# Optimization experiments

Hardware: AMD Instinct MI355X
Metric: run time of the kernel (lower is better)

The kernel has to match this reference:

```python
import jax, jax.numpy as jnp
import numpy as np

V, E, H = 32000, 512, 512  # output_dim, emb_dim, hid_dim
B, S = 256, 128


def setup_inputs() -> dict:
    key = jax.random.key(0)
    ks = jax.random.split(key, 16)
    d = {
        'input_ids': jax.random.randint(ks[0], (B,), 0, V),
        'encoded': jax.random.normal(ks[1], (B, S, 2 * H), jnp.float32),
        'src': jax.random.randint(ks[2], (B, S), 0, V),
        'prev_state': jax.random.normal(ks[3], (B, H), jnp.float32),
        'weighted': jax.random.normal(ks[4], (B, 2 * H), jnp.float32),
        'order': 1,
        # parameters (PyTorch layouts: Linear weight is (out,in); GRU gates order r,z,n)
        'embed_w': jax.random.normal(ks[5], (V, E), jnp.float32) * 0.02,
        'gru_w_ih': jax.random.normal(ks[6], (3 * H, E + 2 * H), jnp.float32) * 0.02,
        'gru_w_hh': jax.random.normal(ks[7], (3 * H, H), jnp.float32) * 0.02,
        'gru_b_ih': jnp.zeros((3 * H,), jnp.float32),
        'gru_b_hh': jnp.zeros((3 * H,), jnp.float32),
        'Ws_w': jax.random.normal(ks[8], (H, 2 * H), jnp.float32) * 0.02,
        'Ws_b': jnp.zeros((H,), jnp.float32),
        'Wo_w': jax.random.normal(ks[9], (V, H), jnp.float32) * 0.02,
        'Wo_b': jnp.zeros((V,), jnp.float32),
        'Wc_w': jax.random.normal(ks[10], (H, 2 * H), jnp.float32) * 0.02,
        'Wc_b': jnp.zeros((H,), jnp.float32),
    }
    return d


def _forward(input_ids, encoded, src, prev_state, weighted, order,
             embed_w, gru_w_ih, gru_w_hh, gru_b_ih, gru_b_hh,
             Ws_w, Ws_b, Wo_w, Wo_b, Wc_w, Wc_b):
    b, s, _ = encoded.shape
    v = Wo_w.shape[0]
    if order == 0:
        prev_state = encoded[:, -1] @ Ws_w.T + Ws_b           # (B,H)
        weighted = jnp.zeros((b, 2 * gru_w_hh.shape[1]), encoded.dtype)
    # GRU cell, single step (seq_len=1), torch gate order r,z,n
    x = jnp.concatenate([embed_w[input_ids], weighted], axis=-1)  # (B, E+2H)
    gi = x @ gru_w_ih.T + gru_b_ih
    gh = prev_state @ gru_w_hh.T + gru_b_hh
    i_r, i_z, i_n = jnp.split(gi, 3, axis=-1)
    h_r, h_z, h_n = jnp.split(gh, 3, axis=-1)
    r = jax.nn.sigmoid(i_r + h_r)
    z = jax.nn.sigmoid(i_z + h_z)
    n = jnp.tanh(i_n + r * h_n)
    hidden = (1.0 - z) * n + z * prev_state                    # (B,H)

    score_g = hidden @ Wo_w.T + Wo_b                           # (B,V)
    score_c = jnp.tanh(encoded @ Wc_w.T + Wc_b)                # (B,S,H)
    score_c = jnp.einsum('bsh,bh->bs', score_c, hidden)        # (B,S)
    mask = (src == 0).astype(encoded.dtype) * -1000.0
    score_c = jnp.tanh(score_c + mask)

    probs = jax.nn.softmax(jnp.concatenate([score_g, score_c], axis=1), axis=1)
    prob_g = probs[:, :v]
    prob_c = probs[:, v:]                                      # (B,S)

    # vectorized scatter-add replacing the nested python loops
    rows = jnp.arange(b)[:, None]
    prob_c_to_g = jnp.zeros((b, v), probs.dtype).at[rows, src].add(prob_c)
    predicted = (prob_g + prob_c_to_g)[:, None, :]             # (B,1,V)

    eq = (src == input_ids[:, None]).astype(encoded.dtype)     # (B,S)
    idx = eq / jnp.maximum(eq.sum(axis=1, keepdims=True), 1.0)
    attn = prob_c * idx                                        # (B,S)
    weighted_out = jnp.einsum('bs,bsd->bd', attn, encoded)     # (B,2H)
    return predicted, hidden, weighted_out


def reference(input_ids, encoded, src, prev_state, weighted, order,
              embed_w, gru_w_ih, gru_w_hh, gru_b_ih, gru_b_hh,
              Ws_w, Ws_b, Wo_w, Wo_b, Wc_w, Wc_b):
    return _forward(input_ids, encoded, src, prev_state, weighted, order,
                    embed_w, gru_w_ih, gru_w_hh, gru_b_ih, gru_b_hh,
                    Ws_w, Ws_b, Wo_w, Wo_b, Wc_w, Wc_b)
```

## Files before the change

kernel.cpp:

```cpp
#include <hip/hip_runtime.h>
#include <cstdint>
#include <cstddef>

#define B_ 256
#define S_ 128
#define H_ 512
#define E_ 512
#define V_ 32000
#define NBLK_G (V_ / 64)

typedef _Float16 half_t;
typedef _Float16 half8 __attribute__((ext_vector_type(8)));
typedef float floatx4 __attribute__((ext_vector_type(4)));

__device__ __forceinline__ float sigmoidf_(float x) { return 1.0f / (1.0f + __expf(-x)); }
__device__ __forceinline__ float fast_tanh(float x) {
    float e = __expf(2.0f * x);
    return 1.0f - 2.0f / (e + 1.0f);
}

__global__ __launch_bounds__(256)
void prep_kernel(const int* __restrict__ ids, const float* __restrict__ encoded,
                 const float* __restrict__ prev_state, const float* __restrict__ weighted,
                 const int* __restrict__ order_p, const float* __restrict__ embed,
                 const float* __restrict__ Ws_w, const float* __restrict__ Ws_b,
                 float* __restrict__ x, float* __restrict__ prev)
{
    int i = blockIdx.x * 256 + threadIdx.x;
    int b = i >> 11;
    int j = i & 2047;
    int order = order_p[0];
    if (j < 1536) {
        float v;
        if (j < 512) v = embed[(size_t)ids[b] * E_ + j];
        else         v = (order == 0) ? 0.0f : weighted[b * 1024 + (j - 512)];
        x[b * 1536 + j] = v;
    } else {
        int h = j - 1536;
        float v;
        if (order != 0) {
            v = prev_state[b * H_ + h];
        } else {
            const float* e  = encoded + ((size_t)b * S_ + (S_ - 1)) * 1024;
            const float* wr = Ws_w + (size_t)h * 1024;
            float accv = Ws_b[h];
            for (int k = 0; k < 1024; ++k) accv += e[k] * wr[k];
            v = accv;
        }
        prev[b * H_ + h] = v;
    }
}

template<int BM, int BN, int WAVES_M, int WAVES_N, int EPI>
__global__ __launch_bounds__(256, 2)
void gemm_f16(const float* __restrict__ A, const float* __restrict__ Bw,
              float* __restrict__ C, const float* __restrict__ bias,
              float* __restrict__ aux, int K, int lda, int ldb, int ldc, int nblk)
{
    constexpr int BK = 32;
    constexpr int WM = BM / WAVES_M;
    constexpr int WN = BN / WAVES_N;
    constexpr int FM = WM / 16;
    constexpr int FN = WN / 16;
    constexpr int A_ITEMS = (BM * 4) / 256;
    constexpr int B_ITEMS = (BN * 4) / 256;

    __shared__ half_t As[BM * BK];
    __shared__ half_t Bs[BN * BK];

    const int tid  = threadIdx.x;
    const int wid  = tid >> 6;
    const int lane = tid & 63;
    const int wm   = wid % WAVES_M;
    const int wn   = wid / WAVES_M;
    const int bm0  = blockIdx.y * BM;
    const int bn0  = blockIdx.x * BN;
    const int col  = lane & 15;
    const int quad = lane >> 4;
    const int swz  = (quad ^ (col & 3)) * 8;

    floatx4 acc[FM][FN] = {};

    for (int kt = 0; kt < K; kt += BK) {
        float4 ar[A_ITEMS][2], br[B_ITEMS][2];
#pragma unroll
        for (int i = 0; i < A_ITEMS; ++i) {
            int idx = tid + i * 256, row = idx >> 2, ch = idx & 3;
            const float* p = A + (size_t)(bm0 + row) * lda + kt + ch * 8;
            ar[i][0] = *(const float4*)p; ar[i][1] = *(const float4*)(p + 4);
        }
#pragma unroll
        for (int i = 0; i < B_ITEMS; ++i) {
            int idx = tid + i * 256, row = idx >> 2, ch = idx & 3;
            const float* p = Bw + (size_t)(bn0 + row) * ldb + kt + ch * 8;
            br[i][0] = *(const float4*)p; br[i][1] = *(const float4*)(p + 4);
        }
        __syncthreads();
#pragma unroll
        for (int i = 0; i < A_ITEMS; ++i) {
            int idx = tid + i * 256, row = idx >> 2, ch = idx & 3;
            int pos = (ch ^ (row & 3)) * 8;
            half8 h;
            h[0] = (half_t)ar[i][0].x; h[1] = (half_t)ar[i][0].y;
            h[2] = (half_t)ar[i][0].z; h[3] = (half_t)ar[i][0].w;
            h[4] = (half_t)ar[i][1].x; h[5] = (half_t)ar[i][1].y;
            h[6] = (half_t)ar[i][1].z; h[7] = (half_t)ar[i][1].w;
            *(half8*)(&As[row * BK + pos]) = h;
        }
#pragma unroll
        for (int i = 0; i < B_ITEMS; ++i) {
            int idx = tid + i * 256, row = idx >> 2, ch = idx & 3;
            int pos = (ch ^ (row & 3)) * 8;
            half8 h;
            h[0] = (half_t)br[i][0].x; h[1] = (half_t)br[i][0].y;
            h[2] = (half_t)br[i][0].z; h[3] = (half_t)br[i][0].w;
            h[4] = (half_t)br[i][1].x; h[5] = (half_t)br[i][1].y;
            h[6] = (half_t)br[i][1].z; h[7] = (half_t)br[i][1].w;
            *(half8*)(&Bs[row * BK + pos]) = h;
        }
        __syncthreads();

        half8 af[FM], bf[FN];
#pragma unroll
        for (int fm = 0; fm < FM; ++fm)
            af[fm] = *(const half8*)(&As[(wm * WM + fm * 16 + col) * BK + swz]);
#pragma unroll
        for (int fn = 0; fn < FN; ++fn)
            bf[fn] = *(const half8*)(&Bs[(wn * WN + fn * 16 + col) * BK + swz]);
#pragma unroll
        for (int fm = 0; fm < FM; ++fm)
#pragma unroll
            for (int fn = 0; fn < FN; ++fn)
                acc[fm][fn] = __builtin_amdgcn_mfma_f32_16x16x32_f16(af[fm], bf[fn], acc[fm][fn], 0, 0, 0);
    }

    if constexpr (EPI == 0) {
#pragma unroll
        for (int fm = 0; fm < FM; ++fm) {
            int m0 = bm0 + wm * WM + fm * 16 + quad * 4;
#pragma unroll
            for (int fn = 0; fn < FN; ++fn) {
                int n = bn0 + wn * WN + fn * 16 + col;
                float bv = bias[n];
#pragma unroll
                for (int r = 0; r < 4; ++r)
                    C[(size_t)(m0 + r) * ldc + n] = acc[fm][fn][r] + bv;
            }
        }
    } else {
        const int bx = blockIdx.x;
#pragma unroll
        for (int fm = 0; fm < FM; ++fm) {
            int m0 = bm0 + wm * WM + fm * 16 + quad * 4;
            float vv[FN][4];
#pragma unroll
            for (int fn = 0; fn < FN; ++fn) {
                int n = bn0 + fn * 16 + col;
                float bv = bias[n];
#pragma unroll
                for (int r = 0; r < 4; ++r) {
                    vv[fn][r] = acc[fm][fn][r] + bv;
                    C[(size_t)(m0 + r) * ldc + n] = vv[fn][r];
                }
            }
#pragma unroll
            for (int r = 0; r < 4; ++r) {
                float mx = vv[0][r];
#pragma unroll
                for (int fn = 1; fn < FN; ++fn) mx = fmaxf(mx, vv[fn][r]);
#pragma unroll
                for (int off = 1; off < 16; off <<= 1)
                    mx = fmaxf(mx, __shfl_xor(mx, off, 64));
                float se = 0.f;
#pragma unroll
                for (int fn = 0; fn < FN; ++fn) se += __expf(vv[fn][r] - mx);
#pragma unroll
                for (int off = 1; off < 16; off <<= 1)
                    se += __shfl_xor(se, off, 64);
                if (col == 0) {
                    aux[(size_t)(m0 + r) * nblk + bx] = mx;
                    aux[(size_t)256 * nblk + (size_t)(m0 + r) * nblk + bx] = se;
                }
            }
        }
    }
}

__global__ __launch_bounds__(512, 2)
void wc_sc_kernel(const float* __restrict__ enc, const float* __restrict__ Wc,
                  const float* __restrict__ bias, const float* __restrict__ hidden,
                  float* __restrict__ sc_out)
{
    constexpr int BK = 32;
    __shared__ half_t As[64 * BK];
    __shared__ half_t Bs[512 * BK];
    __shared__ float  s_part[4 * 64];

    const int tid  = threadIdx.x;
    const int wid  = tid >> 6;
    const int lane = tid & 63;
    const int wm   = wid & 1;
    const int wn   = wid >> 1;
    const int bm0  = blockIdx.x * 64;
    const int col  = lane & 15;
    const int quad = lane >> 4;
    const int swz  = (quad ^ (col & 3)) * 8;

    floatx4 acc[2][8] = {};

    for (int kt = 0; kt < 1024; kt += BK) {
        float4 br[4][2], ar[2];
#pragma unroll
        for (int i = 0; i < 4; ++i) {
            int idx = tid + i * 512, row = idx >> 2, ch = idx & 3;
            const float* p = Wc + (size_t)row * 1024 + kt + ch * 8;
            br[i][0] = *(const float4*)p; br[i][1] = *(const float4*)(p + 4);
        }
        if (tid < 256) {
            int row = tid >> 2, ch = tid & 3;
            const float* p = enc + (size_t)(bm0 + row) * 1024 + kt + ch * 8;
            ar[0] = *(const float4*)p; ar[1] = *(const float4*)(p + 4);
        }
        __syncthreads();
#pragma unroll
        for (int i = 0; i < 4; ++i) {
            int idx = tid + i * 512, row = idx >> 2, ch = idx & 3;
            int pos = (ch ^ (row & 3)) * 8;
            half8 h;
            h[0] = (half_t)br[i][0].x; h[1] = (half_t)br[i][0].y;
            h[2] = (half_t)br[i][0].z; h[3] = (half_t)br[i][0].w;
            h[4] = (half_t)br[i][1].x; h[5] = (half_t)br[i][1].y;
            h[6] = (half_t)br[i][1].z; h[7] = (half_t)br[i][1].w;
            *(half8*)(&Bs[row * BK + pos]) = h;
        }
        if (tid < 256) {
            int row = tid >> 2, ch = tid & 3;
            int pos = (ch ^ (row & 3)) * 8;
            half8 h;
            h[0] = (half_t)ar[0].x; h[1] = (half_t)ar[0].y;
            h[2] = (half_t)ar[0].z; h[3] = (half_t)ar[0].w;
            h[4] = (half_t)ar[1].x; h[5] = (half_t)ar[1].y;
            h[6] = (half_t)ar[1].z; h[7] = (half_t)ar[1].w;
            *(half8*)(&As[row * BK + pos]) = h;
        }
        __syncthreads();

        half8 af[2], bf[8];
#pragma unroll
        for (int fm = 0; fm < 2; ++fm)
            af[fm] = *(const half8*)(&As[(wm * 32 + fm * 16 + col) * BK + swz]);
#pragma unroll
        for (int fn = 0; fn < 8; ++fn)
            bf[fn] = *(const half8*)(&Bs[(wn * 128 + fn * 16 + col) * BK + swz]);
#pragma unroll
        for (int fm = 0; fm < 2; ++fm)
#pragma unroll
            for (int fn = 0; fn < 8; ++fn)
                acc[fm][fn] = __builtin_amdgcn_mfma_f32_16x16x32_f16(af[fm], bf[fn], acc[fm][fn], 0, 0, 0);
    }

    const float* hid = hidden + (size_t)(bm0 >> 7) * H_;
#pragma unroll
    for (int fm = 0; fm < 2; ++fm) {
        float p0 = 0.f, p1 = 0.f, p2 = 0.f, p3 = 0.f;
#pragma unroll
        for (int fn = 0; fn < 8; ++fn) {
            int n = wn * 128 + fn * 16 + col;
            float bv = bias[n];
            float hv = hid[n];
            p0 += fast_tanh(acc[fm][fn][0] + bv) * hv;
            p1 += fast_tanh(acc[fm][fn][1] + bv) * hv;
            p2 += fast_tanh(acc[fm][fn][2] + bv) * hv;
            p3 += fast_tanh(acc[fm][fn][3] + bv) * hv;
        }
#pragma unroll
        for (int off = 1; off < 16; off <<= 1) {
            p0 += __shfl_xor(p0, off, 64);
            p1 += __shfl_xor(p1, off, 64);
            p2 += __shfl_xor(p2, off, 64);
            p3 += __shfl_xor(p3, off, 64);
        }
        if (col == 0) {
            int rloc = wm * 32 + fm * 16 + quad * 4;
            s_part[wn * 64 + rloc + 0] = p0;
            s_part[wn * 64 + rloc + 1] = p1;
            s_part[wn * 64 + rloc + 2] = p2;
            s_part[wn * 64 + rloc + 3] = p3;
        }
    }
    __syncthreads();
    if (tid < 64) {
        float s = s_part[tid] + s_part[64 + tid] + s_part[128 + tid] + s_part[192 + tid];
        sc_out[bm0 + tid] = s;
    }
}

__global__ __launch_bounds__(256)
void gate_kernel(const float* __restrict__ gi, const float* __restrict__ gh,
                 const float* __restrict__ prev, float* __restrict__ hidden)
{
    int i = blockIdx.x * 256 + threadIdx.x;
    int b = i >> 9;
    int h = i & 511;
    const float* gib = gi + (size_t)b * 1536;
    const float* ghb = gh + (size_t)b * 1536;
    float r = sigmoidf_(gib[h] + ghb[h]);
    float z = sigmoidf_(gib[h + 512] + ghb[h + 512]);
    float n = tanhf(gib[h + 1024] + r * ghb[h + 1024]);
    hidden[i] = (1.0f - z) * n + z * prev[i];
}

__global__ __launch_bounds__(256)
void final_kernel(const float* __restrict__ sc_raw,
                  const int* __restrict__ src, const int* __restrict__ ids,
                  const float* __restrict__ encoded, const float* __restrict__ parts,
                  float* __restrict__ predicted, float* __restrict__ weighted_out)
{
    int b = blockIdx.x;
    int t = threadIdx.x;
    __shared__ float s_scf[S_];
    __shared__ float s_attn[S_];
    __shared__ int   s_src[S_];
    __shared__ float rm[4], rs[4];
    __shared__ int   s_cnt;

    float* pred = predicted + (size_t)b * V_;
    const float* pm = parts + (size_t)b * NBLK_G;
    const float* ps = parts + (size_t)256 * NBLK_G + (size_t)b * NBLK_G;

    if (t < S_) {
        int sv = src[b * S_ + t];
        s_src[t] = sv;
        float raw = sc_raw[b * S_ + t];
        if (sv == 0) raw -= 1000.0f;
        s_scf[t] = tanhf(raw);
    }

    float m = -1e30f, s = 0.f;
    for (int j = t; j < NBLK_G; j += 256) {
        float mo = pm[j], so = ps[j];
        float mn = fmaxf(m, mo);
        s = s * __expf(m - mn) + so * __expf(mo - mn);
        m = mn;
    }
    __syncthreads();
    if (t < S_) {
        float x = s_scf[t];
        float mn = fmaxf(m, x);
        s = s * __expf(m - mn) + __expf(x - mn);
        m = mn;
    }
#pragma unroll
    for (int off = 1; off < 64; off <<= 1) {
        float mo = __shfl_xor(m, off, 64);
        float so = __shfl_xor(s, off, 64);
        float mn = fmaxf(m, mo);
        s = s * __expf(m - mn) + so * __expf(mo - mn);
        m = mn;
    }
    if ((t & 63) == 0) { rm[t >> 6] = m; rs[t >> 6] = s; }
    __syncthreads();
    float M = rm[0], Z = rs[0];
#pragma unroll
    for (int w = 1; w < 4; ++w) {
        float mo = rm[w], so = rs[w];
        float mn = fmaxf(M, mo);
        Z = Z * __expf(M - mn) + so * __expf(mo - mn);
        M = mn;
    }
    float invZ = 1.0f / Z;

    float4* pr4 = (float4*)pred;
    for (int i = t; i < V_ / 4; i += 256) {
        float4 x = pr4[i];
        float4 o;
        o.x = __expf(x.x - M) * invZ;
        o.y = __expf(x.y - M) * invZ;
        o.z = __expf(x.z - M) * invZ;
        o.w = __expf(x.w - M) * invZ;
        pr4[i] = o;
    }

    int ii = ids[b];
    if (t == 0) {
        int c = 0;
        for (int s2 = 0; s2 < S_; ++s2) c += (s_src[s2] == ii) ? 1 : 0;
        s_cnt = (c > 0) ? c : 1;
    }
    __syncthreads();

    if (t < S_) {
        float pc = __expf(s_scf[t] - M) * invZ;
        atomicAdd(&pred[s_src[t]], pc);
        s_attn[t] = (s_src[t] == ii) ? pc / (float)s_cnt : 0.f;
    }
    __syncthreads();

    const float* eb = encoded + (size_t)b * S_ * 1024;
    for (int d = t; d < 1024; d += 256) {
        float accv = 0.f;
        for (int s2 = 0; s2 < S_; ++s2) {
            float a = s_attn[s2];
            if (a != 0.f) accv += a * eb[s2 * 1024 + d];
        }
        weighted_out[b * 1024 + d] = accv;
    }
}

extern "C" void kernel_launch(void* const* d_in, const int* in_sizes, int n_in,
                              void* d_out, int out_size, void* d_ws, size_t ws_size,
                              hipStream_t stream)
{
    const int*   input_ids  = (const int*)d_in[0];
    const float* encoded    = (const float*)d_in[1];
    const int*   src        = (const int*)d_in[2];
    const float* prev_state = (const float*)d_in[3];
    const float* weighted   = (const float*)d_in[4];
    const int*   order      = (const int*)d_in[5];
    const float* embed_w    = (const float*)d_in[6];
    const float* gru_w_ih   = (const float*)d_in[7];
    const float* gru_w_hh   = (const float*)d_in[8];
    const float* gru_b_ih   = (const float*)d_in[9];
    const float* gru_b_hh   = (const float*)d_in[10];
    const float* Ws_w       = (const float*)d_in[11];
    const float* Ws_b       = (const float*)d_in[12];
    const float* Wo_w       = (const float*)d_in[13];
    const float* Wo_b       = (const float*)d_in[14];
    const float* Wc_w       = (const float*)d_in[15];
    const float* Wc_b       = (const float*)d_in[16];
    (void)in_sizes; (void)n_in; (void)out_size; (void)ws_size;

    float* predicted    = (float*)d_out;
    float* hidden       = predicted + (size_t)B_ * V_;
    float* weighted_out = hidden + (size_t)B_ * H_;

    char* w = (char*)d_ws;
    float* x_f32  = (float*)w;  w += (size_t)B_ * 1536 * 4;
    float* prev_f = (float*)w;  w += (size_t)B_ * H_ * 4;
    float* gi     = (float*)w;  w += (size_t)B_ * 1536 * 4;
    float* gh     = (float*)w;  w += (size_t)B_ * 1536 * 4;
    float* sc_raw = (float*)w;  w += (size_t)B_ * S_ * 4;
    float* parts  = (float*)w;  w += (size_t)2 * B_ * NBLK_G * 4;

    prep_kernel<<<2048, 256, 0, stream>>>(input_ids, encoded, prev_state, weighted,
                                          order, embed_w, Ws_w, Ws_b, x_f32, prev_f);

    gemm_f16<64, 64, 2, 2, 0><<<dim3(1536 / 64, 256 / 64), 256, 0, stream>>>(
        x_f32, gru_w_ih, gi, gru_b_ih, nullptr, 1536, 1536, 1536, 1536, 0);
    gemm_f16<64, 64, 2, 2, 0><<<dim3(1536 / 64, 256 / 64), 256, 0, stream>>>(
        prev_f, gru_w_hh, gh, gru_b_hh, nullptr, 512, 512, 512, 1536, 0);

    gate_kernel<<<(B_ * H_) / 256, 256, 0, stream>>>(gi, gh, prev_f, hidden);

    wc_sc_kernel<<<(B_ * S_) / 64, 512, 0, stream>>>(encoded, Wc_w, Wc_b, hidden, sc_raw);

    gemm_f16<256, 64, 4, 1, 2><<<dim3(NBLK_G, 1), 256, 0, stream>>>(
        hidden, Wo_w, predicted, Wo_b, parts, 512, 512, 512, V_, NBLK_G);

    final_kernel<<<B_, 256, 0, stream>>>(sc_raw, src, input_ids, encoded, parts,
                                         predicted, weighted_out);
}
```

Baseline: 507.6 us.

## Pre-convert Wc to fp16 and stream B fragments directly into registers in wc_sc

Adds a small kernel that converts Wc to fp16 once per call into workspace. The wc_sc kernel then loads MFMA B fragments straight from global fp16 memory into registers, so the per-tile fp32 load, conversion and LDS staging of the 512-row weight tile go away. Each wave now owns 64 output columns and all 64 rows. The encoder A tile is double-buffered in LDS with register prefetch, and the occupancy hint is raised. The cost is an extra launch, extra workspace, and B reads from global/L2 that are less coalesced.

```diff
diff --git a/kernel.cpp b/kernel.cpp
--- a/kernel.cpp
+++ b/kernel.cpp
@@ -51,6 +51,19 @@
     }
 }
 
+__global__ __launch_bounds__(256)
+void wc_cvt_kernel(const float* __restrict__ Wc, half_t* __restrict__ out)
+{
+    int i = blockIdx.x * 256 + threadIdx.x;
+    const float* p = Wc + (size_t)i * 8;
+    float4 a = *(const float4*)p;
+    float4 b = *(const float4*)(p + 4);
+    half8 h;
+    h[0] = (half_t)a.x; h[1] = (half_t)a.y; h[2] = (half_t)a.z; h[3] = (half_t)a.w;
+    h[4] = (half_t)b.x; h[5] = (half_t)b.y; h[6] = (half_t)b.z; h[7] = (half_t)b.w;
+    *(half8*)(out + (size_t)i * 8) = h;
+}
+
 template<int BM, int BN, int WAVES_M, int WAVES_N, int EPI>
 __global__ __launch_bounds__(256, 2)
 void gemm_f16(const float* __restrict__ A, const float* __restrict__ Bw,
@@ -186,86 +199,99 @@
     }
 }
 
-__global__ __launch_bounds__(512, 2)
-void wc_sc_kernel(const float* __restrict__ enc, const float* __restrict__ Wc,
+__global__ __launch_bounds__(512, 4)
+void wc_sc_kernel(const float* __restrict__ enc, const half_t* __restrict__ WcH,
                   const float* __restrict__ bias, const float* __restrict__ hidden,
                   float* __restrict__ sc_out)
 {
-    constexpr int BK = 32;
-    __shared__ half_t As[64 * BK];
-    __shared__ half_t Bs[512 * BK];
-    __shared__ float  s_part[4 * 64];
+    __shared__ half_t As[2][64 * 32];
+    __shared__ float  s_part[8 * 64];
 
     const int tid  = threadIdx.x;
     const int wid  = tid >> 6;
     const int lane = tid & 63;
-    const int wm   = wid & 1;
-    const int wn   = wid >> 1;
-    const int bm0  = blockIdx.x * 64;
     const int col  = lane & 15;
     const int quad = lane >> 4;
     const int swz  = (quad ^ (col & 3)) * 8;
-
-    floatx4 acc[2][8] = {};
-
-    for (int kt = 0; kt < 1024; kt += BK) {
-        float4 br[4][2], ar[2];
-#pragma unroll
-        for (int i = 0; i < 4; ++i) {
-            int idx = tid + i * 512, row = idx >> 2, ch = idx & 3;
-            const float* p = Wc + (size_t)row * 1024 + kt + ch * 8;
-            br[i][0] = *(const float4*)p; br[i][1] = *(const float4*)(p + 4);
-        }
+    const int bm0  = blockIdx.x * 64;
+
+    const int ar_row = tid >> 2;
+    const int ar_ch  = tid & 3;
+    const float* aptr = enc + (size_t)(bm0 + ar_row) * 1024 + ar_ch * 8;
+    const int a_pos = ar_row * 32 + (ar_ch ^ (ar_row & 3)) * 8;
+
+    const half_t* bptr0 = WcH + (size_t)(wid * 64 +  0 + col) * 1024 + quad * 8;
+    const half_t* bptr1 = WcH + (size_t)(wid * 64 + 16 + col) * 1024 + quad * 8;
+    const half_t* bptr2 = WcH + (size_t)(wid * 64 + 32 + col) * 1024 + quad * 8;
+    const half_t* bptr3 = WcH + (size_t)(wid * 64 + 48 + col) * 1024 + quad * 8;
+
+    floatx4 acc[4][4] = {};
+    float4 ar0, ar1;
+    half8 bf0[4], bf1[4];
+
+    if (tid < 256) { ar0 = *(const float4*)(aptr); ar1 = *(const float4*)(aptr + 4); }
+    bf0[0] = *(const half8*)(bptr0);
+    bf0[1] = *(const half8*)(bptr1);
+    bf0[2] = *(const half8*)(bptr2);
+    bf0[3] = *(const half8*)(bptr3);
+
+    for (int t2 = 0; t2 < 16; ++t2) {
+        const int kA = t2 * 64;
         if (tid < 256) {
-            int row = tid >> 2, ch = tid & 3;
-            const float* p = enc + (size_t)(bm0 + row) * 1024 + kt + ch * 8;
-            ar[0] = *(const float4*)p; ar[1] = *(const float4*)(p + 4);
+            half8 h;
+            h[0] = (half_t)ar0.x; h[1] = (half_t)ar0.y; h[2] = (half_t)ar0.z; h[3] = (half_t)ar0.w;
+            h[4] = (half_t)ar1.x; h[5] = (half_t)ar1.y; h[6] = (half_t)ar1.z; h[7] = (half_t)ar1.w;
+            *(half8*)(&As[0][a_pos]) = h;
         }
         __syncthreads();
-#pragma unroll
-        for (int i = 0; i < 4; ++i) {
-            int idx = tid + i * 512, row = idx >> 2, ch = idx & 3;
-            int pos = (ch ^ (row & 3)) * 8;
+        if (tid < 256) {
+            ar0 = *(const float4*)(aptr + kA + 32);
+            ar1 = *(const float4*)(aptr + kA + 36);
+        }
+        bf1[0] = *(const half8*)(bptr0 + kA + 32);
+        bf1[1] = *(const half8*)(bptr1 + kA + 32);
+        bf1[2] = *(const half8*)(bptr2 + kA + 32);
+        bf1[3] = *(const half8*)(bptr3 + kA + 32);
+#pragma unroll
+        for (int fm = 0; fm < 4; ++fm) {
+            half8 af = *(const half8*)(&As[0][(fm * 16 + col) * 32 + swz]);
+#pragma unroll
+            for (int fn = 0; fn < 4; ++fn)
+                acc[fm][fn] = __builtin_amdgcn_mfma_f32_16x16x32_f16(af, bf0[fn], acc[fm][fn], 0, 0, 0);
+        }
+        if (tid < 256) {
             half8 h;
-            h[0] = (half_t)br[i][0].x; h[1] = (half_t)br[i][0].y;
-            h[2] = (half_t)br[i][0].z; h[3] = (half_t)br[i][0].w;
-            h[4] = (half_t)br[i][1].x; h[5] = (half_t)br[i][1].y;
-            h[6] = (half_t)br[i][1].z; h[7] = (half_t)br[i][1].w;
-            *(half8*)(&Bs[row * BK + pos]) = h;
-        }
-        if (tid < 256) {
-            int row = tid >> 2, ch = tid & 3;
-            int pos = (ch ^ (row & 3)) * 8;
-            half8 h;
-            h[0] = (half_t)ar[0].x; h[1] = (half_t)ar[0].y;
-            h[2] = (half_t)ar[0].z; h[3] = (half_t)ar[0].w;
-            h[4] = (half_t)ar[1].x; h[5] = (half_t)ar[1].y;
-            h[6] = (half_t)ar[1].z; h[7] = (half_t)ar[1].w;
-            *(half8*)(&As[row * BK + pos]) = h;
+            h[0] = (half_t)ar0.x; h[1] = (half_t)ar0.y; h[2] = (half_t)ar0.z; h[3] = (half_t)ar0.w;
+            h[4] = (half_t)ar1.x; h[5] = (half_t)ar1.y; h[6] = (half_t)ar1.z; h[7] = (half_t)ar1.w;
+            *(half8*)(&As[1][a_pos]) = h;
         }
         __syncthreads();
-
-        half8 af[2], bf[8];
-#pragma unroll
-        for (int fm = 0; fm < 2; ++fm)
-            af[fm] = *(const half8*)(&As[(wm * 32 + fm * 16 + col) * BK + swz]);
-#pragma unroll
-        for (int fn = 0; fn < 8; ++fn)
-            bf[fn] = *(const half8*)(&Bs[(wn * 128 + fn * 16 + col) * BK + swz]);
-#pragma unroll
-        for (int fm = 0; fm < 2; ++fm)
-#pragma unroll
-            for (int fn = 0; fn < 8; ++fn)
-                acc[fm][fn] = __builtin_amdgcn_mfma_f32_16x16x32_f16(af[fm], bf[fn], acc[fm][fn], 0, 0, 0);
+        if (kA + 64 < 1024) {
+            if (tid < 256) {
+                ar0 = *(const float4*)(aptr + kA + 64);
+                ar1 = *(const float4*)(aptr + kA + 68);
+            }
+            bf0[0] = *(const half8*)(bptr0 + kA + 64);
+            bf0[1] = *(const half8*)(bptr1 + kA + 64);
+            bf0[2] = *(const half8*)(bptr2 + kA + 64);
+            bf0[3] = *(const half8*)(bptr3 + kA + 64);
+        }
+#pragma unroll
+        for (int fm = 0; fm < 4; ++fm) {
+            half8 af = *(const half8*)(&As[1][(fm * 16 + col) * 32 + swz]);
+#pragma unroll
+            for (int fn = 0; fn < 4; ++fn)
+                acc[fm][fn] = __builtin_amdgcn_mfma_f32_16x16x32_f16(af, bf1[fn], acc[fm][fn], 0, 0, 0);
+        }
     }
 
     const float* hid = hidden + (size_t)(bm0 >> 7) * H_;
 #pragma unroll
-    for (int fm = 0; fm < 2; ++fm) {
+    for (int fm = 0; fm < 4; ++fm) {
         float p0 = 0.f, p1 = 0.f, p2 = 0.f, p3 = 0.f;
 #pragma unroll
-        for (int fn = 0; fn < 8; ++fn) {
-            int n = wn * 128 + fn * 16 + col;
+        for (int fn = 0; fn < 4; ++fn) {
+            int n = wid * 64 + fn * 16 + col;
             float bv = bias[n];
             float hv = hid[n];
             p0 += fast_tanh(acc[fm][fn][0] + bv) * hv;
@@ -281,16 +307,18 @@
             p3 += __shfl_xor(p3, off, 64);
         }
         if (col == 0) {
-            int rloc = wm * 32 + fm * 16 + quad * 4;
-            s_part[wn * 64 + rloc + 0] = p0;
-            s_part[wn * 64 + rloc + 1] = p1;
-            s_part[wn * 64 + rloc + 2] = p2;
-            s_part[wn * 64 + rloc + 3] = p3;
+            int rloc = fm * 16 + quad * 4;
+            s_part[wid * 64 + rloc + 0] = p0;
+            s_part[wid * 64 + rloc + 1] = p1;
+            s_part[wid * 64 + rloc + 2] = p2;
+            s_part[wid * 64 + rloc + 3] = p3;
         }
     }
     __syncthreads();
     if (tid < 64) {
-        float s = s_part[tid] + s_part[64 + tid] + s_part[128 + tid] + s_part[192 + tid];
+        float s = 0.f;
+#pragma unroll
+        for (int w = 0; w < 8; ++w) s += s_part[w * 64 + tid];
         sc_out[bm0 + tid] = s;
     }
 }
@@ -441,6 +469,9 @@
     float* gh     = (float*)w;  w += (size_t)B_ * 1536 * 4;
     float* sc_raw = (float*)w;  w += (size_t)B_ * S_ * 4;
     float* parts  = (float*)w;  w += (size_t)2 * B_ * NBLK_G * 4;
+    half_t* wc_h  = (half_t*)w; w += (size_t)H_ * 1024 * 2;
+
+    wc_cvt_kernel<<<256, 256, 0, stream>>>(Wc_w, wc_h);
 
     prep_kernel<<<2048, 256, 0, stream>>>(input_ids, encoded, prev_state, weighted,
                                           order, embed_w, Ws_w, Ws_b, x_f32, prev_f);
@@ -452,7 +483,7 @@
 
     gate_kernel<<<(B_ * H_) / 256, 256, 0, stream>>>(gi, gh, prev_f, hidden);
 
-    wc_sc_kernel<<<(B_ * S_) / 64, 512, 0, stream>>>(encoded, Wc_w, Wc_b, hidden, sc_raw);
+    wc_sc_kernel<<<(B_ * S_) / 64, 512, 0, stream>>>(encoded, wc_h, Wc_b, hidden, sc_raw);
 
     gemm_f16<256, 64, 4, 1, 2><<<dim3(NBLK_G, 1), 256, 0, stream>>>(
         hidden, Wo_w, predicted, Wo_b, parts, 512, 512, 512, V_, NBLK_G);
```

New measurement: 473.5 us. 6.7% less time.
